# Performance work log

Measured on AMD Instinct MI355X. Metric: run time of the kernel, lower is better.

The kernel has to match this reference:

```python
import jax, jax.numpy as jnp
import numpy as np

EPS = 1e-12
B, C, H, M, E, P = 2, 20000, 64, 8, 200000, 3


def setup_inputs() -> dict:
    key = jax.random.key(0)
    ks = jax.random.split(key, 24)
    inp = {}
    inp["features"] = jax.random.normal(ks[0], (B, C, H), jnp.float32)
    inp["positions"] = jax.random.normal(ks[1], (B, C, P), jnp.float32)
    inp["edge_index"] = jax.random.randint(ks[2], (2, E), 0, C)
    inp["degree"] = jax.random.randint(ks[3], (C,), 1, 33).astype(jnp.float32)
    inp["cell_node_indices"] = jax.random.randint(ks[4], (C, M), 0, C)
    mask = (jax.random.uniform(ks[5], (C, M)) > 0.3).astype(jnp.float32)
    inp["cell_node_mask"] = mask.at[:, 0].set(1.0)  # first node always valid (pad semantics)

    def lin(k, fan_in, fan_out):
        return (jax.random.normal(k, (fan_in, fan_out), jnp.float32) / np.sqrt(fan_in)).astype(jnp.float32)

    # message MLP: Linear(2H+4 -> H), SiLU, Linear(H -> H)
    inp["W1"] = lin(ks[6], 2 * H + 4, H); inp["b1"] = jnp.zeros((H,), jnp.float32)
    inp["W2"] = lin(ks[7], H, H);         inp["b2"] = jnp.zeros((H,), jnp.float32)
    # position MLP: Linear(H -> H), SiLU, Linear(H -> 1)
    inp["P1"] = lin(ks[8], H, H);  inp["pb1"] = jnp.zeros((H,), jnp.float32)
    inp["P2"] = lin(ks[9], H, 1);  inp["pb2"] = jnp.zeros((1,), jnp.float32)
    # update MLP: Linear(2H -> H), SiLU, Linear(H -> H)
    inp["U1"] = lin(ks[10], 2 * H, H); inp["ub1"] = jnp.zeros((H,), jnp.float32)
    inp["U2"] = lin(ks[11], H, H);     inp["ub2"] = jnp.zeros((H,), jnp.float32)
    return inp


def _mlp(x, Wa, ba, Wb, bb):
    return jax.nn.silu(x @ Wa + ba) @ Wb + bb


def _forward(features, positions, edge_index, degree, cell_node_indices, cell_node_mask,
             W1, b1, W2, b2, P1, pb1, P2, pb2, U1, ub1, U2, ub2):
    src, dst = edge_index[0], edge_index[1]
    # gather padded node positions per cell: [B, C, M, P]
    node_pos = positions[:, cell_node_indices]

    h_src = features[:, src]                      # [B,E,H]
    h_dst = features[:, dst]
    rel = positions[:, src] - positions[:, dst]   # [B,E,P]
    dist = jnp.linalg.norm(rel, axis=-1, keepdims=True)  # [B,E,1]

    sp = node_pos[:, src]                         # [B,E,M,P]
    dp = node_pos[:, dst]
    mx = cell_node_mask[src]                      # [E,M]
    my = cell_node_mask[dst]

    # pairwise distances [B,E,M,M] via gram trick (avoids [B,E,M,M,P] intermediate)
    sp2 = jnp.sum(sp * sp, -1)                    # [B,E,M]
    dp2 = jnp.sum(dp * dp, -1)
    cross = jnp.einsum('bemp,benp->bemn', sp, dp)
    d = jnp.sqrt(jnp.maximum(sp2[..., :, None] + dp2[..., None, :] - 2.0 * cross, 0.0) + EPS)

    # masked pairwise-distance sum
    w = mx[:, :, None] * my[:, None, :]           # [E,M,M]
    pairwise = jnp.sum(d * w[None], axis=(-1, -2))  # [B,E]

    # centroid distance
    denx = jnp.maximum(mx.sum(-1, keepdims=True), EPS)  # [E,1]
    deny = jnp.maximum(my.sum(-1, keepdims=True), EPS)
    cx = jnp.sum(sp * mx[None, :, :, None], axis=2) / denx[None]  # [B,E,P]
    cy = jnp.sum(dp * my[None, :, :, None], axis=2) / deny[None]
    centroid = jnp.linalg.norm(cx - cy, axis=-1)  # [B,E]

    # Hausdorff distance (masked min/max)
    inf = jnp.float32(jnp.inf)
    d_xy = jnp.where(my[None, :, None, :] <= 0, inf, d)
    min_xy = jnp.where(mx[None] <= 0, 0.0, d_xy.min(-1))  # [B,E,M]
    h_xy = min_xy.max(-1)                                  # [B,E]
    d_yx = jnp.where(mx[None, :, None, :] <= 0, inf, jnp.swapaxes(d, -1, -2))
    min_yx = jnp.where(my[None] <= 0, 0.0, d_yx.min(-1))
    h_yx = min_yx.max(-1)
    haus = jnp.maximum(h_xy, h_yx)

    invariants = jnp.concatenate([dist, pairwise[..., None], centroid[..., None], haus[..., None]], -1)  # [B,E,4]
    msg_in = jnp.concatenate([h_src, h_dst, invariants], -1)  # [B,E,2H+4]
    messages = _mlp(msg_in, W1, b1, W2, b2)                   # [B,E,H]

    # scatter-aggregate into destination cells, degree-normalize
    agg = jnp.zeros_like(features).at[:, dst].add(messages)
    agg = agg / jnp.maximum(degree, 1.0)[None, :, None]

    # position update
    wts = jnp.tanh(_mlp(messages, P1, pb1, P2, pb2))          # [B,E,1]
    pos_upd = jnp.zeros_like(positions).at[:, dst].add(wts * rel)

    new_features = features + _mlp(jnp.concatenate([features, agg], -1), U1, ub1, U2, ub2)
    new_positions = positions + pos_upd
    return new_features, new_positions


def reference(features, positions, edge_index, degree, cell_node_indices, cell_node_mask,
              W1, b1, W2, b2, P1, pb1, P2, pb2, U1, ub1, U2, ub2):
    return _forward(features, positions, edge_index, degree, cell_node_indices, cell_node_mask,
                    W1, b1, W2, b2, P1, pb1, P2, pb2, U1, ub1, U2, ub2)
```

## Files before the change

kernel.cpp:

```cpp
#include <hip/hip_runtime.h>
#include <hip/hip_bf16.h>

#define B_ 2
#define C_ 20000
#define H_ 64
#define M_ 8
#define E_ 200000
#define P_ 3
#define EPS_ 1e-12f
#define ET_ (E_ / 64)

typedef __attribute__((ext_vector_type(8))) short short8;
typedef __attribute__((ext_vector_type(4))) float float4v;

__device__ __forceinline__ float silu_(float x) {
    return x / (1.f + __expf(-x));
}
__device__ __forceinline__ unsigned short f2b(float f) {
    unsigned u = __float_as_uint(f);
    unsigned r = (u + 0x7FFF + ((u >> 16) & 1)) >> 16;
    return (unsigned short)r;
}
__device__ __forceinline__ float b2f(unsigned short h) {
    return __uint_as_float(((unsigned)h) << 16);
}
__device__ __forceinline__ unsigned pk2u(float a, float b) {
    __hip_bfloat162 h = __float22bfloat162_rn(make_float2(a, b));
    unsigned u; __builtin_memcpy(&u, &h, sizeof(u)); return u;
}

#define W1S_OFF 0
#define W2S_OFF 8192
#define P1S_OFF 12288
#define U1S_OFF 16384
#define U2S_OFF 24576
#define WBUF_ELEMS 28672

#define NB_PREP  120
#define NB_FEATB 2500
#define NB_DESC  157
#define NB_HIST  782
#define NB_COMBO (NB_PREP + NB_FEATB + NB_DESC + NB_HIST)

__global__ __launch_bounds__(256) void combo_kernel(
    const float* __restrict__ W1, const float* __restrict__ W2,
    const float* __restrict__ P1, const float* __restrict__ U1,
    const float* __restrict__ U2, unsigned short* __restrict__ wbuf,
    const float* __restrict__ feat, unsigned short* __restrict__ featb,
    const float* __restrict__ pos, const int* __restrict__ cni,
    const float* __restrict__ mask, float* __restrict__ desc,
    const int* __restrict__ ei, int* __restrict__ cnt)
{
    const int bid = blockIdx.x;
    if (bid < NB_PREP) {
        int t = bid * 256 + threadIdx.x;
        if (t >= WBUF_ELEMS) return;
        const float* W; int e;
        if (t < W2S_OFF)      { W = W1; e = t; }
        else if (t < U1S_OFF) { W = (t < P1S_OFF) ? W2 : P1; e = (t < P1S_OFF) ? t - W2S_OFF : t - P1S_OFF; }
        else if (t < U2S_OFF) { W = U1; e = t - U1S_OFF; }
        else                  { W = U2; e = t - U2S_OFF; }
        int j = e & 7, lane = (e >> 3) & 63, nt = (e >> 9) & 3, kk = e >> 11;
        int k = kk * 32 + ((lane >> 4) * 8) + j;
        int n = nt * 16 + (lane & 15);
        wbuf[t] = f2b(W[k * 64 + n]);
    } else if (bid < NB_PREP + NB_FEATB) {
        int t = (bid - NB_PREP) * 256 + threadIdx.x;
        float4 v = *(const float4*)&feat[(size_t)t * 4];
        *(uint2*)&featb[(size_t)t * 4] = make_uint2(pk2u(v.x, v.y), pk2u(v.z, v.w));
    } else if (bid < NB_PREP + NB_FEATB + NB_DESC) {
        int tid = (bid - NB_PREP - NB_FEATB) * 256 + threadIdx.x;
        if (tid >= B_ * C_) return;
        int b = tid / C_, c = tid - b * C_;
        const float* pb = pos + (size_t)b * C_ * P_;
        float4* D = (float4*)(desc + (size_t)tid * 40);
        int4 n0 = *(const int4*)&cni[c*8];
        int4 n1 = *(const int4*)&cni[c*8 + 4];
        float4 m0 = *(const float4*)&mask[c*8];
        float4 m1 = *(const float4*)&mask[c*8 + 4];
        int ni[8] = {n0.x, n0.y, n0.z, n0.w, n1.x, n1.y, n1.z, n1.w};
        float mm[8] = {m0.x, m0.y, m0.z, m0.w, m1.x, m1.y, m1.z, m1.w};
        float sx = 0.f, sy = 0.f, sz = 0.f, sm = 0.f;
        #pragma unroll
        for (int m = 0; m < 8; ++m) {
            float x = pb[ni[m]*3+0], y = pb[ni[m]*3+1], z = pb[ni[m]*3+2];
            D[m] = make_float4(x, y, z, mm[m]);
            sx += x * mm[m]; sy += y * mm[m]; sz += z * mm[m]; sm += mm[m];
        }
        float inv = 1.f / fmaxf(sm, EPS_);
        D[8] = make_float4(sx * inv, sy * inv, sz * inv, sm);
        D[9] = make_float4(pb[c*3+0], pb[c*3+1], pb[c*3+2], 0.f);
    } else {
        int e = (bid - NB_PREP - NB_FEATB - NB_DESC) * 256 + threadIdx.x;
        if (e >= E_) return;
        atomicAdd(&cnt[ei[E_ + e]], 1);
    }
}

__global__ __launch_bounds__(256) void alloc_kernel(
    const int* __restrict__ cnt, int* __restrict__ cursor, int* __restrict__ total)
{
    int idx = blockIdx.x * 256 + threadIdx.x;
    int lane = threadIdx.x & 63;
    int v = (idx < C_) ? cnt[idx] : 0;
    int inc = v;
    #pragma unroll
    for (int s = 1; s < 64; s <<= 1) {
        int n = __shfl_up(inc, s);
        if (lane >= s) inc += n;
    }
    int wtot = __shfl(inc, 63);
    int base = 0;
    if (lane == 0) base = atomicAdd(total, wtot);
    base = __shfl(base, 0);
    if (idx < C_) cursor[idx] = base + inc - v;
}

__global__ __launch_bounds__(256) void scatter_kernel(
    const int* __restrict__ ei, int* __restrict__ cursor,
    int* __restrict__ ssrc, int* __restrict__ sdst)
{
    int e = blockIdx.x * 256 + threadIdx.x;
    if (e >= E_) return;
    int s = ei[e], d = ei[E_ + e];
    int slot = atomicAdd(&cursor[d], 1);
    ssrc[slot] = s;
    sdst[slot] = d;
}

__global__ __launch_bounds__(256) void edge_kernel(
    const unsigned short* __restrict__ featb,
    const int* __restrict__ ssrc, const int* __restrict__ sdst,
    const float* __restrict__ desc,
    const unsigned short* __restrict__ wbuf, const float* __restrict__ W1,
    const float* __restrict__ b1, const float* __restrict__ b2,
    const float* __restrict__ pb1, const float* __restrict__ P2,
    const float* __restrict__ pb2,
    float* __restrict__ aggf, float* __restrict__ out_pos)
{
    __shared__ unsigned short lds[4 * 3328];

    const int tid  = threadIdx.x;
    const int w    = tid >> 6;
    const int lane = tid & 63;
    const int q    = lane >> 4;
    const int l16  = lane & 15;
    const int w16  = w * 16;

    const int tile = blockIdx.x;
    const int b    = tile / ET_;
    const int i0   = (tile - b * ET_) * 64;
    const int s_l  = ssrc[i0 + lane];
    const int d_l  = sdst[i0 + lane];
    const unsigned short* fb = featb + (size_t)b * C_ * H_;

    unsigned short* Xw = lds + w * 3328;
    unsigned short* Hw = Xw + 2176;
    unsigned short* Mw = Xw;

    const int sg = __shfl(s_l, w16 + l16);
    const int dg = __shfl(d_l, w16 + l16);
    const float4* Ds = (const float4*)(desc + ((size_t)b * C_ + sg) * 40);
    const float4* Dd = (const float4*)(desc + ((size_t)b * C_ + dg) * 40);

    float4 S[8];
    float sp2[8], rowmin[8];
    const float INFV = __builtin_inff();
    #pragma unroll
    for (int i = 0; i < 8; ++i) {
        S[i] = Ds[i];
        sp2[i] = S[i].x*S[i].x + S[i].y*S[i].y + S[i].z*S[i].z;
        rowmin[i] = INFV;
    }
    float pair = 0.f, hyx = 0.f;
    #pragma unroll
    for (int jj = 0; jj < 2; ++jj) {
        float4 Dj = Dd[q*2 + jj];
        float dp2 = Dj.x*Dj.x + Dj.y*Dj.y + Dj.z*Dj.z;
        float colmin = INFV;
        #pragma unroll
        for (int i = 0; i < 8; ++i) {
            float cr = S[i].x*Dj.x + S[i].y*Dj.y + S[i].z*Dj.z;
            float dd = sqrtf(fmaxf(sp2[i] + dp2 - 2.f*cr, 0.f) + EPS_);
            pair += dd * S[i].w * Dj.w;
            rowmin[i] = (Dj.w  > 0.f) ? fminf(rowmin[i], dd) : rowmin[i];
            colmin    = (S[i].w > 0.f) ? fminf(colmin, dd)    : colmin;
        }
        hyx = fmaxf(hyx, (Dj.w > 0.f) ? colmin : 0.f);
    }
    pair += __shfl_xor(pair, 16);  pair += __shfl_xor(pair, 32);
    hyx = fmaxf(hyx, __shfl_xor(hyx, 16));  hyx = fmaxf(hyx, __shfl_xor(hyx, 32));
    #pragma unroll
    for (int i = 0; i < 8; ++i) {
        rowmin[i] = fminf(rowmin[i], __shfl_xor(rowmin[i], 16));
        rowmin[i] = fminf(rowmin[i], __shfl_xor(rowmin[i], 32));
    }
    float hxy = 0.f;
    #pragma unroll
    for (int i = 0; i < 8; ++i)
        hxy = fmaxf(hxy, (S[i].w > 0.f) ? rowmin[i] : 0.f);
    float4 Sc = Ds[8], Dc = Dd[8];
    float cdx = Sc.x - Dc.x, cdy = Sc.y - Dc.y, cdz = Sc.z - Dc.z;
    float4 Sp = Ds[9], Dp = Dd[9];
    const float relx = Sp.x - Dp.x, rely = Sp.y - Dp.y, relz = Sp.z - Dp.z;
    const float ivx = sqrtf(relx*relx + rely*rely + relz*relz);
    const float ivy = pair;
    const float ivz = sqrtf(cdx*cdx + cdy*cdy + cdz*cdz);
    const float ivw = fmaxf(hxy, hyx);

    const int rr4 = lane >> 4, c4 = lane & 15;
    #pragma unroll
    for (int it = 0; it < 4; ++it) {
        int rloc = it * 4 + rr4;
        int r = w16 + rloc;
        int sr = __shfl(s_l, r);
        int dr = __shfl(d_l, r);
        uint2 vs = *(const uint2*)&fb[(size_t)sr * 64 + c4 * 4];
        uint2 vd = *(const uint2*)&fb[(size_t)dr * 64 + c4 * 4];
        *(uint2*)&Xw[rloc*136 + c4*4]      = vs;
        *(uint2*)&Xw[rloc*136 + 64 + c4*4] = vd;
    }

    float4v acc[4];
    #pragma unroll
    for (int nt = 0; nt < 4; ++nt) {
        float bv = b1[nt*16 + l16];
        acc[nt] = (float4v){bv, bv, bv, bv};
    }
    #pragma unroll
    for (int kk = 0; kk < 4; ++kk) {
        short8 a = *(const short8*)&Xw[l16*136 + kk*32 + q*8];
        #pragma unroll
        for (int nt = 0; nt < 4; ++nt) {
            short8 bf = *(const short8*)&wbuf[W1S_OFF + (((kk*4 + nt)*64) + lane) * 8];
            acc[nt] = __builtin_amdgcn_mfma_f32_16x16x32_bf16(a, bf, acc[nt], 0, 0, 0);
        }
    }
    float4 iv[4];
    #pragma unroll
    for (int i = 0; i < 4; ++i) {
        int r = q*4 + i;
        iv[i] = make_float4(__shfl(ivx, r), __shfl(ivy, r),
                            __shfl(ivz, r), __shfl(ivw, r));
    }
    #pragma unroll
    for (int nt = 0; nt < 4; ++nt) {
        float wa = W1[128*64 + nt*16 + l16];
        float wb = W1[129*64 + nt*16 + l16];
        float wc = W1[130*64 + nt*16 + l16];
        float wd = W1[131*64 + nt*16 + l16];
        #pragma unroll
        for (int i = 0; i < 4; ++i)
            acc[nt][i] += iv[i].x*wa + iv[i].y*wb + iv[i].z*wc + iv[i].w*wd;
    }
    #pragma unroll
    for (int nt = 0; nt < 4; ++nt)
        #pragma unroll
        for (int i = 0; i < 4; ++i)
            Hw[(q*4 + i)*72 + nt*16 + l16] = f2b(silu_(acc[nt][i]));

    float4v mac[4];
    #pragma unroll
    for (int nt = 0; nt < 4; ++nt) {
        float bv = b2[nt*16 + l16];
        mac[nt] = (float4v){bv, bv, bv, bv};
    }
    #pragma unroll
    for (int kk = 0; kk < 2; ++kk) {
        short8 a = *(const short8*)&Hw[l16*72 + kk*32 + q*8];
        #pragma unroll
        for (int nt = 0; nt < 4; ++nt) {
            short8 bf = *(const short8*)&wbuf[W2S_OFF + (((kk*4 + nt)*64) + lane) * 8];
            mac[nt] = __builtin_amdgcn_mfma_f32_16x16x32_bf16(a, bf, mac[nt], 0, 0, 0);
        }
    }
    #pragma unroll
    for (int nt = 0; nt < 4; ++nt)
        #pragma unroll
        for (int i = 0; i < 4; ++i)
            Mw[(q*4 + i)*72 + nt*16 + l16] = f2b(mac[nt][i]);

    float4v gac[4];
    #pragma unroll
    for (int nt = 0; nt < 4; ++nt) {
        float bv = pb1[nt*16 + l16];
        gac[nt] = (float4v){bv, bv, bv, bv};
    }
    #pragma unroll
    for (int kk = 0; kk < 2; ++kk) {
        short8 a = *(const short8*)&Mw[l16*72 + kk*32 + q*8];
        #pragma unroll
        for (int nt = 0; nt < 4; ++nt) {
            short8 bf = *(const short8*)&wbuf[P1S_OFF + (((kk*4 + nt)*64) + lane) * 8];
            gac[nt] = __builtin_amdgcn_mfma_f32_16x16x32_bf16(a, bf, gac[nt], 0, 0, 0);
        }
    }
    float p2v[4];
    #pragma unroll
    for (int nt = 0; nt < 4; ++nt) p2v[nt] = P2[nt*16 + l16];
    const float pb2v = pb2[0];

    #pragma unroll
    for (int i = 0; i < 4; ++i) {
        float p = 0.f;
        #pragma unroll
        for (int nt = 0; nt < 4; ++nt) p += silu_(gac[nt][i]) * p2v[nt];
        p += __shfl_xor(p, 8);
        p += __shfl_xor(p, 4);
        p += __shfl_xor(p, 2);
        p += __shfl_xor(p, 1);
        float wt = tanhf(p + pb2v);
        if (l16 == 0) *(float*)&Mw[(q*4 + i)*72 + 64] = wt;
    }

    float mrow[16];
    #pragma unroll
    for (int rr = 0; rr < 16; ++rr) mrow[rr] = b2f(Mw[rr*72 + lane]);
    float wtl = *(const float*)&Mw[l16*72 + 64];

    float* aggB = aggf + (size_t)b * C_ * 64;
    float* opB  = out_pos + (size_t)b * C_ * 3;

    int dprev = __shfl(d_l, w16);
    float colacc = 0.f, pxa = 0.f, pya = 0.f, pza = 0.f;
    #pragma unroll
    for (int rr = 0; rr < 16; ++rr) {
        int dcur = __shfl(d_l, w16 + rr);
        if (dcur != dprev) {
            atomicAdd(&aggB[(size_t)dprev * 64 + lane], colacc);
            if (lane < 3) {
                float v = (lane == 0) ? pxa : (lane == 1) ? pya : pza;
                atomicAdd(&opB[(size_t)dprev * 3 + lane], v);
            }
            colacc = 0.f; pxa = 0.f; pya = 0.f; pza = 0.f;
            dprev = dcur;
        }
        float wt = __shfl(wtl, rr);
        colacc += mrow[rr];
        pxa += wt * __shfl(relx, rr);
        pya += wt * __shfl(rely, rr);
        pza += wt * __shfl(relz, rr);
    }
    atomicAdd(&aggB[(size_t)dprev * 64 + lane], colacc);
    if (lane < 3) {
        float v = (lane == 0) ? pxa : (lane == 1) ? pya : pza;
        atomicAdd(&opB[(size_t)dprev * 3 + lane], v);
    }
}

__global__ __launch_bounds__(256) void node_kernel(
    const float* __restrict__ feat, const unsigned short* __restrict__ featb,
    const float* __restrict__ aggf, const float* __restrict__ deg,
    const unsigned short* __restrict__ wbuf,
    const float* __restrict__ ub1, const float* __restrict__ ub2,
    float* __restrict__ out_feat)
{
    __shared__ unsigned short lds[4 * 3328];

    const int tid  = threadIdx.x;
    const int w    = tid >> 6;
    const int lane = tid & 63;
    const int q    = lane >> 4;
    const int l16  = lane & 15;
    const int g0   = blockIdx.x * 64;

    unsigned short* Xw = lds + w * 3328;
    unsigned short* Hw = Xw + 2176;

    const int rr4 = lane >> 4, c4 = lane & 15;
    #pragma unroll
    for (int it = 0; it < 4; ++it) {
        int rloc = it * 4 + rr4;
        int g = g0 + w*16 + rloc;
        int gc = (g >= C_) ? g - C_ : g;
        float sc = 1.f / fmaxf(deg[gc], 1.f);
        uint2  vf = *(const uint2*)&featb[(size_t)g * 64 + c4 * 4];
        float4 va = *(const float4*)&aggf[(size_t)g * 64 + c4 * 4];
        *(uint2*)&Xw[rloc*136 + c4*4]      = vf;
        *(uint2*)&Xw[rloc*136 + 64 + c4*4] =
            make_uint2(pk2u(va.x*sc, va.y*sc), pk2u(va.z*sc, va.w*sc));
    }

    float4v acc[4];
    #pragma unroll
    for (int nt = 0; nt < 4; ++nt) {
        float bv = ub1[nt*16 + l16];
        acc[nt] = (float4v){bv, bv, bv, bv};
    }
    #pragma unroll
    for (int kk = 0; kk < 4; ++kk) {
        short8 a = *(const short8*)&Xw[l16*136 + kk*32 + q*8];
        #pragma unroll
        for (int nt = 0; nt < 4; ++nt) {
            short8 bf = *(const short8*)&wbuf[U1S_OFF + (((kk*4 + nt)*64) + lane) * 8];
            acc[nt] = __builtin_amdgcn_mfma_f32_16x16x32_bf16(a, bf, acc[nt], 0, 0, 0);
        }
    }
    #pragma unroll
    for (int nt = 0; nt < 4; ++nt)
        #pragma unroll
        for (int i = 0; i < 4; ++i)
            Hw[(q*4 + i)*72 + nt*16 + l16] = f2b(silu_(acc[nt][i]));

    float4v oac[4];
    #pragma unroll
    for (int nt = 0; nt < 4; ++nt) {
        float bv = ub2[nt*16 + l16];
        oac[nt] = (float4v){bv, bv, bv, bv};
    }
    #pragma unroll
    for (int kk = 0; kk < 2; ++kk) {
        short8 a = *(const short8*)&Hw[l16*72 + kk*32 + q*8];
        #pragma unroll
        for (int nt = 0; nt < 4; ++nt) {
            short8 bf = *(const short8*)&wbuf[U2S_OFF + (((kk*4 + nt)*64) + lane) * 8];
            oac[nt] = __builtin_amdgcn_mfma_f32_16x16x32_bf16(a, bf, oac[nt], 0, 0, 0);
        }
    }
    #pragma unroll
    for (int nt = 0; nt < 4; ++nt)
        #pragma unroll
        for (int i = 0; i < 4; ++i) {
            size_t idx = (size_t)(g0 + w*16 + q*4 + i) * 64 + nt*16 + l16;
            out_feat[idx] = feat[idx] + oac[nt][i];
        }
}

extern "C" void kernel_launch(void* const* d_in, const int* in_sizes, int n_in,
                              void* d_out, int out_size, void* d_ws, size_t ws_size,
                              hipStream_t stream) {
    const float* feat = (const float*)d_in[0];
    const float* pos  = (const float*)d_in[1];
    const int*   ei   = (const int*)d_in[2];
    const float* deg  = (const float*)d_in[3];
    const int*   cni  = (const int*)d_in[4];
    const float* mask = (const float*)d_in[5];
    const float* W1   = (const float*)d_in[6];
    const float* b1   = (const float*)d_in[7];
    const float* W2   = (const float*)d_in[8];
    const float* b2   = (const float*)d_in[9];
    const float* P1   = (const float*)d_in[10];
    const float* pb1  = (const float*)d_in[11];
    const float* P2   = (const float*)d_in[12];
    const float* pb2  = (const float*)d_in[13];
    const float* U1   = (const float*)d_in[14];
    const float* ub1  = (const float*)d_in[15];
    const float* U2   = (const float*)d_in[16];
    const float* ub2  = (const float*)d_in[17];

    float* out_feat = (float*)d_out;
    float* out_pos  = out_feat + (size_t)B_ * C_ * H_;

    float* desc = (float*)d_ws;
    float* aggf = desc + (size_t)B_ * C_ * 40;
    unsigned short* featb = (unsigned short*)(aggf + (size_t)B_ * C_ * 64);
    unsigned short* wbuf  = featb + (size_t)B_ * C_ * 64;
    int* cnt    = (int*)(wbuf + WBUF_ELEMS);
    int* total  = cnt + C_;
    int* cursor = total + 1;
    int* ssrc   = cursor + C_;
    int* sdst   = ssrc + E_;

    hipMemsetAsync(cnt, 0, (C_ + 1) * sizeof(int), stream);
    hipMemsetAsync(aggf, 0, (size_t)B_ * C_ * 64 * sizeof(float), stream);
    hipMemcpyAsync(out_pos, pos, (size_t)B_ * C_ * P_ * sizeof(float),
                   hipMemcpyDeviceToDevice, stream);

    combo_kernel<<<NB_COMBO, 256, 0, stream>>>(
        W1, W2, P1, U1, U2, wbuf, feat, featb, pos, cni, mask, desc, ei, cnt);

    alloc_kernel<<<(C_ + 255) / 256, 256, 0, stream>>>(cnt, cursor, total);
    scatter_kernel<<<(E_ + 255) / 256, 256, 0, stream>>>(ei, cursor, ssrc, sdst);

    edge_kernel<<<B_ * ET_, 256, 0, stream>>>(
        featb, ssrc, sdst, desc, wbuf, W1, b1, b2, pb1, P2, pb2, aggf, out_pos);

    node_kernel<<<(B_ * C_) / 64, 256, 0, stream>>>(
        feat, featb, aggf, deg, wbuf, ub1, ub2, out_feat);
}
```

Before: 226.5 us.

## Give each wave its own 64-edge tile in the edge kernel

New measurement: 331.2 us. 1.46x slower.

```diff
diff --git a/kernel.cpp b/kernel.cpp
--- a/kernel.cpp
+++ b/kernel.cpp
@@ -8,7 +8,6 @@
 #define E_ 200000
 #define P_ 3
 #define EPS_ 1e-12f
-#define ET_ (E_ / 64)
 
 typedef __attribute__((ext_vector_type(8))) short short8;
 typedef __attribute__((ext_vector_type(4))) float float4v;
@@ -36,11 +35,11 @@
 #define U2S_OFF 24576
 #define WBUF_ELEMS 28672
 
-#define NB_PREP  120
-#define NB_FEATB 2500
-#define NB_DESC  157
-#define NB_HIST  782
-#define NB_COMBO (NB_PREP + NB_FEATB + NB_DESC + NB_HIST)
+#define NB_PREP   120
+#define NB_FEATB  2500
+#define NB_DESC   157
+#define NB_HIST   782
+#define NB_COMBO  (NB_PREP + NB_FEATB + NB_DESC + NB_HIST)
 
 __global__ __launch_bounds__(256) void combo_kernel(
     const float* __restrict__ W1, const float* __restrict__ W2,
@@ -118,19 +117,18 @@
 
 __global__ __launch_bounds__(256) void scatter_kernel(
     const int* __restrict__ ei, int* __restrict__ cursor,
-    int* __restrict__ ssrc, int* __restrict__ sdst)
+    int2* __restrict__ sedge)
 {
     int e = blockIdx.x * 256 + threadIdx.x;
     if (e >= E_) return;
     int s = ei[e], d = ei[E_ + e];
     int slot = atomicAdd(&cursor[d], 1);
-    ssrc[slot] = s;
-    sdst[slot] = d;
-}
-
-__global__ __launch_bounds__(256) void edge_kernel(
+    sedge[slot] = make_int2(s, d);
+}
+
+__global__ __launch_bounds__(128, 4) void edge_kernel(
     const unsigned short* __restrict__ featb,
-    const int* __restrict__ ssrc, const int* __restrict__ sdst,
+    const int2* __restrict__ sedge,
     const float* __restrict__ desc,
     const unsigned short* __restrict__ wbuf, const float* __restrict__ W1,
     const float* __restrict__ b1, const float* __restrict__ b2,
@@ -138,62 +136,59 @@
     const float* __restrict__ pb2,
     float* __restrict__ aggf, float* __restrict__ out_pos)
 {
-    __shared__ unsigned short lds[4 * 3328];
+    __shared__ __align__(16) unsigned short lds[2 * 4352];
 
     const int tid  = threadIdx.x;
     const int w    = tid >> 6;
     const int lane = tid & 63;
     const int q    = lane >> 4;
     const int l16  = lane & 15;
-    const int w16  = w * 16;
-
-    const int tile = blockIdx.x;
-    const int b    = tile / ET_;
-    const int i0   = (tile - b * ET_) * 64;
-    const int s_l  = ssrc[i0 + lane];
-    const int d_l  = sdst[i0 + lane];
+
+    const int wid  = blockIdx.x * 2 + w;
+    const int b    = wid / (E_ / 64);
+    const int i0   = (wid - b * (E_ / 64)) * 64;
+
+    const int2 sd  = sedge[i0 + lane];
+    const int s_l  = sd.x;
+    const int d_l  = sd.y;
     const unsigned short* fb = featb + (size_t)b * C_ * H_;
 
-    unsigned short* Xw = lds + w * 3328;
+    unsigned short* Xw = lds + w * 4352;
     unsigned short* Hw = Xw + 2176;
     unsigned short* Mw = Xw;
-
-    const int sg = __shfl(s_l, w16 + l16);
-    const int dg = __shfl(d_l, w16 + l16);
-    const float4* Ds = (const float4*)(desc + ((size_t)b * C_ + sg) * 40);
-    const float4* Dd = (const float4*)(desc + ((size_t)b * C_ + dg) * 40);
-
-    float4 S[8];
-    float sp2[8], rowmin[8];
+    float* IVw = (float*)(Xw + 3328);
+
+    const float4* Ds = (const float4*)(desc + ((size_t)b * C_ + s_l) * 40);
+    const float4* Dd = (const float4*)(desc + ((size_t)b * C_ + d_l) * 40);
     const float INFV = __builtin_inff();
+    float4 S[8], D[8];
+    #pragma unroll
+    for (int i = 0; i < 8; ++i) { S[i] = Ds[i]; D[i] = Dd[i]; }
+    float a_i[8], infm_i[8], rowmin[8];
     #pragma unroll
     for (int i = 0; i < 8; ++i) {
-        S[i] = Ds[i];
-        sp2[i] = S[i].x*S[i].x + S[i].y*S[i].y + S[i].z*S[i].z;
+        a_i[i] = S[i].x*S[i].x + S[i].y*S[i].y + S[i].z*S[i].z + EPS_;
+        infm_i[i] = (S[i].w > 0.f) ? 0.f : INFV;
         rowmin[i] = INFV;
     }
     float pair = 0.f, hyx = 0.f;
     #pragma unroll
-    for (int jj = 0; jj < 2; ++jj) {
-        float4 Dj = Dd[q*2 + jj];
+    for (int j = 0; j < 8; ++j) {
+        float4 Dj = D[j];
         float dp2 = Dj.x*Dj.x + Dj.y*Dj.y + Dj.z*Dj.z;
-        float colmin = INFV;
+        float infm_j = (Dj.w > 0.f) ? 0.f : INFV;
+        float colmin = INFV, psum = 0.f;
         #pragma unroll
         for (int i = 0; i < 8; ++i) {
             float cr = S[i].x*Dj.x + S[i].y*Dj.y + S[i].z*Dj.z;
-            float dd = sqrtf(fmaxf(sp2[i] + dp2 - 2.f*cr, 0.f) + EPS_);
-            pair += dd * S[i].w * Dj.w;
-            rowmin[i] = (Dj.w  > 0.f) ? fminf(rowmin[i], dd) : rowmin[i];
-            colmin    = (S[i].w > 0.f) ? fminf(colmin, dd)    : colmin;
-        }
+            float t  = (a_i[i] + dp2) - 2.f*cr;
+            float dd = sqrtf(fmaxf(t, EPS_));
+            psum = fmaf(dd, S[i].w, psum);
+            rowmin[i] = fminf(rowmin[i], dd + infm_j);
+            colmin    = fminf(colmin,    dd + infm_i[i]);
+        }
+        pair = fmaf(Dj.w, psum, pair);
         hyx = fmaxf(hyx, (Dj.w > 0.f) ? colmin : 0.f);
-    }
-    pair += __shfl_xor(pair, 16);  pair += __shfl_xor(pair, 32);
-    hyx = fmaxf(hyx, __shfl_xor(hyx, 16));  hyx = fmaxf(hyx, __shfl_xor(hyx, 32));
-    #pragma unroll
-    for (int i = 0; i < 8; ++i) {
-        rowmin[i] = fminf(rowmin[i], __shfl_xor(rowmin[i], 16));
-        rowmin[i] = fminf(rowmin[i], __shfl_xor(rowmin[i], 32));
     }
     float hxy = 0.f;
     #pragma unroll
@@ -203,148 +198,144 @@
     float cdx = Sc.x - Dc.x, cdy = Sc.y - Dc.y, cdz = Sc.z - Dc.z;
     float4 Sp = Ds[9], Dp = Dd[9];
     const float relx = Sp.x - Dp.x, rely = Sp.y - Dp.y, relz = Sp.z - Dp.z;
-    const float ivx = sqrtf(relx*relx + rely*rely + relz*relz);
-    const float ivy = pair;
-    const float ivz = sqrtf(cdx*cdx + cdy*cdy + cdz*cdz);
-    const float ivw = fmaxf(hxy, hyx);
-
-    const int rr4 = lane >> 4, c4 = lane & 15;
-    #pragma unroll
-    for (int it = 0; it < 4; ++it) {
-        int rloc = it * 4 + rr4;
-        int r = w16 + rloc;
-        int sr = __shfl(s_l, r);
-        int dr = __shfl(d_l, r);
-        uint2 vs = *(const uint2*)&fb[(size_t)sr * 64 + c4 * 4];
-        uint2 vd = *(const uint2*)&fb[(size_t)dr * 64 + c4 * 4];
-        *(uint2*)&Xw[rloc*136 + c4*4]      = vs;
-        *(uint2*)&Xw[rloc*136 + 64 + c4*4] = vd;
-    }
-
-    float4v acc[4];
+    {
+        float ivx = sqrtf(relx*relx + rely*rely + relz*relz);
+        float ivz = sqrtf(cdx*cdx + cdy*cdy + cdz*cdz);
+        float ivw = fmaxf(hxy, hyx);
+        *(float4*)&IVw[lane*8]     = make_float4(ivx, pair, ivz, ivw);
+        *(float4*)&IVw[lane*8 + 4] = make_float4(relx, rely, relz, 0.f);
+    }
+
+    float b1v[4], b2v[4], pb1v[4], p2v[4];
+    float wta[4], wtb[4], wtc[4], wtd[4];
     #pragma unroll
     for (int nt = 0; nt < 4; ++nt) {
-        float bv = b1[nt*16 + l16];
-        acc[nt] = (float4v){bv, bv, bv, bv};
-    }
-    #pragma unroll
-    for (int kk = 0; kk < 4; ++kk) {
-        short8 a = *(const short8*)&Xw[l16*136 + kk*32 + q*8];
-        #pragma unroll
-        for (int nt = 0; nt < 4; ++nt) {
-            short8 bf = *(const short8*)&wbuf[W1S_OFF + (((kk*4 + nt)*64) + lane) * 8];
-            acc[nt] = __builtin_amdgcn_mfma_f32_16x16x32_bf16(a, bf, acc[nt], 0, 0, 0);
-        }
-    }
-    float4 iv[4];
-    #pragma unroll
-    for (int i = 0; i < 4; ++i) {
-        int r = q*4 + i;
-        iv[i] = make_float4(__shfl(ivx, r), __shfl(ivy, r),
-                            __shfl(ivz, r), __shfl(ivw, r));
-    }
-    #pragma unroll
-    for (int nt = 0; nt < 4; ++nt) {
-        float wa = W1[128*64 + nt*16 + l16];
-        float wb = W1[129*64 + nt*16 + l16];
-        float wc = W1[130*64 + nt*16 + l16];
-        float wd = W1[131*64 + nt*16 + l16];
-        #pragma unroll
-        for (int i = 0; i < 4; ++i)
-            acc[nt][i] += iv[i].x*wa + iv[i].y*wb + iv[i].z*wc + iv[i].w*wd;
-    }
-    #pragma unroll
-    for (int nt = 0; nt < 4; ++nt)
-        #pragma unroll
-        for (int i = 0; i < 4; ++i)
-            Hw[(q*4 + i)*72 + nt*16 + l16] = f2b(silu_(acc[nt][i]));
-
-    float4v mac[4];
-    #pragma unroll
-    for (int nt = 0; nt < 4; ++nt) {
-        float bv = b2[nt*16 + l16];
-        mac[nt] = (float4v){bv, bv, bv, bv};
-    }
-    #pragma unroll
-    for (int kk = 0; kk < 2; ++kk) {
-        short8 a = *(const short8*)&Hw[l16*72 + kk*32 + q*8];
-        #pragma unroll
-        for (int nt = 0; nt < 4; ++nt) {
-            short8 bf = *(const short8*)&wbuf[W2S_OFF + (((kk*4 + nt)*64) + lane) * 8];
-            mac[nt] = __builtin_amdgcn_mfma_f32_16x16x32_bf16(a, bf, mac[nt], 0, 0, 0);
-        }
-    }
-    #pragma unroll
-    for (int nt = 0; nt < 4; ++nt)
-        #pragma unroll
-        for (int i = 0; i < 4; ++i)
-            Mw[(q*4 + i)*72 + nt*16 + l16] = f2b(mac[nt][i]);
-
-    float4v gac[4];
-    #pragma unroll
-    for (int nt = 0; nt < 4; ++nt) {
-        float bv = pb1[nt*16 + l16];
-        gac[nt] = (float4v){bv, bv, bv, bv};
-    }
-    #pragma unroll
-    for (int kk = 0; kk < 2; ++kk) {
-        short8 a = *(const short8*)&Mw[l16*72 + kk*32 + q*8];
-        #pragma unroll
-        for (int nt = 0; nt < 4; ++nt) {
-            short8 bf = *(const short8*)&wbuf[P1S_OFF + (((kk*4 + nt)*64) + lane) * 8];
-            gac[nt] = __builtin_amdgcn_mfma_f32_16x16x32_bf16(a, bf, gac[nt], 0, 0, 0);
-        }
-    }
-    float p2v[4];
-    #pragma unroll
-    for (int nt = 0; nt < 4; ++nt) p2v[nt] = P2[nt*16 + l16];
+        b1v[nt]  = b1[nt*16 + l16];
+        b2v[nt]  = b2[nt*16 + l16];
+        pb1v[nt] = pb1[nt*16 + l16];
+        p2v[nt]  = P2[nt*16 + l16];
+        wta[nt]  = W1[128*64 + nt*16 + l16];
+        wtb[nt]  = W1[129*64 + nt*16 + l16];
+        wtc[nt]  = W1[130*64 + nt*16 + l16];
+        wtd[nt]  = W1[131*64 + nt*16 + l16];
+    }
     const float pb2v = pb2[0];
-
-    #pragma unroll
-    for (int i = 0; i < 4; ++i) {
-        float p = 0.f;
-        #pragma unroll
-        for (int nt = 0; nt < 4; ++nt) p += silu_(gac[nt][i]) * p2v[nt];
-        p += __shfl_xor(p, 8);
-        p += __shfl_xor(p, 4);
-        p += __shfl_xor(p, 2);
-        p += __shfl_xor(p, 1);
-        float wt = tanhf(p + pb2v);
-        if (l16 == 0) *(float*)&Mw[(q*4 + i)*72 + 64] = wt;
-    }
-
-    float mrow[16];
-    #pragma unroll
-    for (int rr = 0; rr < 16; ++rr) mrow[rr] = b2f(Mw[rr*72 + lane]);
-    float wtl = *(const float*)&Mw[l16*72 + 64];
 
     float* aggB = aggf + (size_t)b * C_ * 64;
     float* opB  = out_pos + (size_t)b * C_ * 3;
-
-    int dprev = __shfl(d_l, w16);
-    float colacc = 0.f, pxa = 0.f, pya = 0.f, pza = 0.f;
-    #pragma unroll
-    for (int rr = 0; rr < 16; ++rr) {
-        int dcur = __shfl(d_l, w16 + rr);
-        if (dcur != dprev) {
-            atomicAdd(&aggB[(size_t)dprev * 64 + lane], colacc);
-            if (lane < 3) {
-                float v = (lane == 0) ? pxa : (lane == 1) ? pya : pza;
-                atomicAdd(&opB[(size_t)dprev * 3 + lane], v);
+    const int rr4 = lane >> 4, c4 = lane & 15;
+
+    for (int it = 0; it < 4; ++it) {
+        #pragma unroll
+        for (int it2 = 0; it2 < 4; ++it2) {
+            int rloc = it2 * 4 + rr4;
+            int sr = __shfl(s_l, it*16 + rloc);
+            int dr = __shfl(d_l, it*16 + rloc);
+            *(uint2*)&Xw[rloc*136 + c4*4]      = *(const uint2*)&fb[(size_t)sr*64 + c4*4];
+            *(uint2*)&Xw[rloc*136 + 64 + c4*4] = *(const uint2*)&fb[(size_t)dr*64 + c4*4];
+        }
+
+        float4v acc[4];
+        #pragma unroll
+        for (int nt = 0; nt < 4; ++nt)
+            acc[nt] = (float4v){b1v[nt], b1v[nt], b1v[nt], b1v[nt]};
+        #pragma unroll
+        for (int kk = 0; kk < 4; ++kk) {
+            short8 a = *(const short8*)&Xw[l16*136 + kk*32 + q*8];
+            #pragma unroll
+            for (int nt = 0; nt < 4; ++nt) {
+                short8 bf = *(const short8*)&wbuf[W1S_OFF + (((kk*4 + nt)*64) + lane) * 8];
+                acc[nt] = __builtin_amdgcn_mfma_f32_16x16x32_bf16(a, bf, acc[nt], 0, 0, 0);
             }
-            colacc = 0.f; pxa = 0.f; pya = 0.f; pza = 0.f;
-            dprev = dcur;
-        }
-        float wt = __shfl(wtl, rr);
-        colacc += mrow[rr];
-        pxa += wt * __shfl(relx, rr);
-        pya += wt * __shfl(rely, rr);
-        pza += wt * __shfl(relz, rr);
-    }
-    atomicAdd(&aggB[(size_t)dprev * 64 + lane], colacc);
-    if (lane < 3) {
-        float v = (lane == 0) ? pxa : (lane == 1) ? pya : pza;
-        atomicAdd(&opB[(size_t)dprev * 3 + lane], v);
+        }
+        #pragma unroll
+        for (int i = 0; i < 4; ++i) {
+            float4 iv = *(const float4*)&IVw[(it*16 + q*4 + i) * 8];
+            #pragma unroll
+            for (int nt = 0; nt < 4; ++nt)
+                acc[nt][i] += iv.x*wta[nt] + iv.y*wtb[nt] + iv.z*wtc[nt] + iv.w*wtd[nt];
+        }
+        #pragma unroll
+        for (int nt = 0; nt < 4; ++nt)
+            #pragma unroll
+            for (int i = 0; i < 4; ++i)
+                Hw[(q*4 + i)*72 + nt*16 + l16] = f2b(silu_(acc[nt][i]));
+
+        float4v mac[4];
+        #pragma unroll
+        for (int nt = 0; nt < 4; ++nt)
+            mac[nt] = (float4v){b2v[nt], b2v[nt], b2v[nt], b2v[nt]};
+        #pragma unroll
+        for (int kk = 0; kk < 2; ++kk) {
+            short8 a = *(const short8*)&Hw[l16*72 + kk*32 + q*8];
+            #pragma unroll
+            for (int nt = 0; nt < 4; ++nt) {
+                short8 bf = *(const short8*)&wbuf[W2S_OFF + (((kk*4 + nt)*64) + lane) * 8];
+                mac[nt] = __builtin_amdgcn_mfma_f32_16x16x32_bf16(a, bf, mac[nt], 0, 0, 0);
+            }
+        }
+        #pragma unroll
+        for (int nt = 0; nt < 4; ++nt)
+            #pragma unroll
+            for (int i = 0; i < 4; ++i)
+                Mw[(q*4 + i)*72 + nt*16 + l16] = f2b(mac[nt][i]);
+
+        float4v gac[4];
+        #pragma unroll
+        for (int nt = 0; nt < 4; ++nt)
+            gac[nt] = (float4v){pb1v[nt], pb1v[nt], pb1v[nt], pb1v[nt]};
+        #pragma unroll
+        for (int kk = 0; kk < 2; ++kk) {
+            short8 a = *(const short8*)&Mw[l16*72 + kk*32 + q*8];
+            #pragma unroll
+            for (int nt = 0; nt < 4; ++nt) {
+                short8 bf = *(const short8*)&wbuf[P1S_OFF + (((kk*4 + nt)*64) + lane) * 8];
+                gac[nt] = __builtin_amdgcn_mfma_f32_16x16x32_bf16(a, bf, gac[nt], 0, 0, 0);
+            }
+        }
+        #pragma unroll
+        for (int i = 0; i < 4; ++i) {
+            float p = 0.f;
+            #pragma unroll
+            for (int nt = 0; nt < 4; ++nt) p += silu_(gac[nt][i]) * p2v[nt];
+            p += __shfl_xor(p, 8);
+            p += __shfl_xor(p, 4);
+            p += __shfl_xor(p, 2);
+            p += __shfl_xor(p, 1);
+            float wt = tanhf(p + pb2v);
+            if (l16 == 0) *(float*)&Mw[(q*4 + i)*72 + 64] = wt;
+        }
+
+        float mrow[16];
+        #pragma unroll
+        for (int rr = 0; rr < 16; ++rr) mrow[rr] = b2f(Mw[rr*72 + lane]);
+        float wtl = *(const float*)&Mw[l16*72 + 64];
+
+        int dprev = __shfl(d_l, it*16);
+        float colacc = 0.f, pxa = 0.f, pya = 0.f, pza = 0.f;
+        #pragma unroll
+        for (int rr = 0; rr < 16; ++rr) {
+            int dcur = __shfl(d_l, it*16 + rr);
+            if (dcur != dprev) {
+                atomicAdd(&aggB[(size_t)dprev * 64 + lane], colacc);
+                if (lane < 3) {
+                    float v = (lane == 0) ? pxa : (lane == 1) ? pya : pza;
+                    atomicAdd(&opB[(size_t)dprev * 3 + lane], v);
+                }
+                colacc = 0.f; pxa = 0.f; pya = 0.f; pza = 0.f;
+                dprev = dcur;
+            }
+            float wt = __shfl(wtl, rr);
+            colacc += mrow[rr];
+            pxa = fmaf(wt, __shfl(relx, it*16 + rr), pxa);
+            pya = fmaf(wt, __shfl(rely, it*16 + rr), pya);
+            pza = fmaf(wt, __shfl(relz, it*16 + rr), pza);
+        }
+        atomicAdd(&aggB[(size_t)dprev * 64 + lane], colacc);
+        if (lane < 3) {
+            float v = (lane == 0) ? pxa : (lane == 1) ? pya : pza;
+            atomicAdd(&opB[(size_t)dprev * 3 + lane], v);
+        }
     }
 }
 
@@ -458,8 +449,7 @@
     int* cnt    = (int*)(wbuf + WBUF_ELEMS);
     int* total  = cnt + C_;
     int* cursor = total + 1;
-    int* ssrc   = cursor + C_;
-    int* sdst   = ssrc + E_;
+    int2* sedge = (int2*)(cursor + C_);
 
     hipMemsetAsync(cnt, 0, (C_ + 1) * sizeof(int), stream);
     hipMemsetAsync(aggf, 0, (size_t)B_ * C_ * 64 * sizeof(float), stream);
@@ -470,10 +460,10 @@
         W1, W2, P1, U1, U2, wbuf, feat, featb, pos, cni, mask, desc, ei, cnt);
 
     alloc_kernel<<<(C_ + 255) / 256, 256, 0, stream>>>(cnt, cursor, total);
-    scatter_kernel<<<(E_ + 255) / 256, 256, 0, stream>>>(ei, cursor, ssrc, sdst);
-
-    edge_kernel<<<B_ * ET_, 256, 0, stream>>>(
-        featb, ssrc, sdst, desc, wbuf, W1, b1, b2, pb1, P2, pb2, aggf, out_pos);
+    scatter_kernel<<<(E_ + 255) / 256, 256, 0, stream>>>(ei, cursor, sedge);
+
+    edge_kernel<<<(B_ * E_) / 128, 128, 0, stream>>>(
+        featb, sedge, desc, wbuf, W1, b1, b2, pb1, P2, pb2, aggf, out_pos);
 
     node_kernel<<<(B_ * C_) / 64, 256, 0, stream>>>(
         feat, featb, aggf, deg, wbuf, ub1, ub2, out_feat);
```

## Split edge geometry into a separate per-edge kernel and fuse memset/copy into it

Applied to the files above, without the earlier changes.

Result: slower. 247.3 us (+9.2%).

```diff
diff --git a/kernel.cpp b/kernel.cpp
--- a/kernel.cpp
+++ b/kernel.cpp
@@ -16,6 +16,10 @@
 __device__ __forceinline__ float silu_(float x) {
     return x / (1.f + __expf(-x));
 }
+__device__ __forceinline__ float tanh_fast_(float x) {
+    float ex = __expf(2.f * x);
+    return 1.f - 2.f / (ex + 1.f);
+}
 __device__ __forceinline__ unsigned short f2b(float f) {
     unsigned u = __float_as_uint(f);
     unsigned r = (u + 0x7FFF + ((u >> 16) & 1)) >> 16;
@@ -36,11 +40,16 @@
 #define U2S_OFF 24576
 #define WBUF_ELEMS 28672
 
-#define NB_PREP  120
-#define NB_FEATB 2500
-#define NB_DESC  157
-#define NB_HIST  782
-#define NB_COMBO (NB_PREP + NB_FEATB + NB_DESC + NB_HIST)
+#define NB_PREP   120
+#define NB_FEATB  2500
+#define NB_DESC   157
+#define NB_HIST   782
+#define NB_COMBO  (NB_PREP + NB_FEATB + NB_DESC + NB_HIST)
+
+#define NB_GEOM   3125
+#define NB_AGGZ   2500
+#define NB_PCPY   118
+#define NB_GEOMK  (NB_GEOM + NB_AGGZ + NB_PCPY)
 
 __global__ __launch_bounds__(256) void combo_kernel(
     const float* __restrict__ W1, const float* __restrict__ W2,
@@ -118,20 +127,85 @@
 
 __global__ __launch_bounds__(256) void scatter_kernel(
     const int* __restrict__ ei, int* __restrict__ cursor,
-    int* __restrict__ ssrc, int* __restrict__ sdst)
+    int2* __restrict__ sedge)
 {
     int e = blockIdx.x * 256 + threadIdx.x;
     if (e >= E_) return;
     int s = ei[e], d = ei[E_ + e];
     int slot = atomicAdd(&cursor[d], 1);
-    ssrc[slot] = s;
-    sdst[slot] = d;
+    sedge[slot] = make_int2(s, d);
+}
+
+__global__ __launch_bounds__(256) void geom_kernel(
+    const int2* __restrict__ sedge, const float* __restrict__ desc,
+    float* __restrict__ inv8,
+    float* __restrict__ aggf, const float* __restrict__ pos,
+    float* __restrict__ out_pos)
+{
+    const int bid = blockIdx.x;
+    if (bid >= NB_GEOM) {
+        if (bid < NB_GEOM + NB_AGGZ) {
+            int t = (bid - NB_GEOM) * 256 + threadIdx.x;
+            ((float4*)aggf)[t] = make_float4(0.f, 0.f, 0.f, 0.f);
+        } else {
+            int t = (bid - NB_GEOM - NB_AGGZ) * 256 + threadIdx.x;
+            if (t < (B_ * C_ * P_) / 4)
+                ((float4*)out_pos)[t] = ((const float4*)pos)[t];
+        }
+        return;
+    }
+    int gid = bid * 256 + threadIdx.x;
+    int b = gid / E_, i = gid - b * E_;
+    int2 sd = sedge[i];
+    const float4* Ds = (const float4*)(desc + ((size_t)b * C_ + sd.x) * 40);
+    const float4* Dd = (const float4*)(desc + ((size_t)b * C_ + sd.y) * 40);
+    const float INFV = __builtin_inff();
+    float4 S[8];
+    float a_i[8], infm_i[8], rowmin[8];
+    #pragma unroll
+    for (int k = 0; k < 8; ++k) {
+        S[k] = Ds[k];
+        a_i[k] = S[k].x*S[k].x + S[k].y*S[k].y + S[k].z*S[k].z + EPS_;
+        infm_i[k] = (S[k].w > 0.f) ? 0.f : INFV;
+        rowmin[k] = INFV;
+    }
+    float pair = 0.f, hyx = 0.f;
+    #pragma unroll
+    for (int j = 0; j < 8; ++j) {
+        float4 Dj = Dd[j];
+        float dp2 = Dj.x*Dj.x + Dj.y*Dj.y + Dj.z*Dj.z;
+        float infm_j = (Dj.w > 0.f) ? 0.f : INFV;
+        float colmin = INFV, psum = 0.f;
+        #pragma unroll
+        for (int k = 0; k < 8; ++k) {
+            float cr = S[k].x*Dj.x + S[k].y*Dj.y + S[k].z*Dj.z;
+            float t  = (a_i[k] + dp2) - 2.f*cr;
+            float dd = sqrtf(fmaxf(t, EPS_));
+            psum = fmaf(dd, S[k].w, psum);
+            rowmin[k] = fminf(rowmin[k], dd + infm_j);
+            colmin    = fminf(colmin,    dd + infm_i[k]);
+        }
+        pair = fmaf(Dj.w, psum, pair);
+        hyx = fmaxf(hyx, (Dj.w > 0.f) ? colmin : 0.f);
+    }
+    float hxy = 0.f;
+    #pragma unroll
+    for (int k = 0; k < 8; ++k)
+        hxy = fmaxf(hxy, (S[k].w > 0.f) ? rowmin[k] : 0.f);
+    float4 Sc = Ds[8], Dc = Dd[8];
+    float cdx = Sc.x - Dc.x, cdy = Sc.y - Dc.y, cdz = Sc.z - Dc.z;
+    float4 Sp = Ds[9], Dp = Dd[9];
+    float relx = Sp.x - Dp.x, rely = Sp.y - Dp.y, relz = Sp.z - Dp.z;
+    float dist = sqrtf(relx*relx + rely*rely + relz*relz);
+    float cen  = sqrtf(cdx*cdx + cdy*cdy + cdz*cdz);
+    float haus = fmaxf(hxy, hyx);
+    ((float4*)inv8)[(size_t)gid * 2]     = make_float4(dist, pair, cen, haus);
+    ((float4*)inv8)[(size_t)gid * 2 + 1] = make_float4(relx, rely, relz, 0.f);
 }
 
 __global__ __launch_bounds__(256) void edge_kernel(
     const unsigned short* __restrict__ featb,
-    const int* __restrict__ ssrc, const int* __restrict__ sdst,
-    const float* __restrict__ desc,
+    const int2* __restrict__ sedge, const float* __restrict__ inv8,
     const unsigned short* __restrict__ wbuf, const float* __restrict__ W1,
     const float* __restrict__ b1, const float* __restrict__ b2,
     const float* __restrict__ pb1, const float* __restrict__ P2,
@@ -150,63 +224,18 @@
     const int tile = blockIdx.x;
     const int b    = tile / ET_;
     const int i0   = (tile - b * ET_) * 64;
-    const int s_l  = ssrc[i0 + lane];
-    const int d_l  = sdst[i0 + lane];
+    const int2 sd  = sedge[i0 + lane];
+    const int s_l  = sd.x;
+    const int d_l  = sd.y;
     const unsigned short* fb = featb + (size_t)b * C_ * H_;
+    const float* ivb = inv8 + ((size_t)b * E_ + i0) * 8;
 
     unsigned short* Xw = lds + w * 3328;
     unsigned short* Hw = Xw + 2176;
     unsigned short* Mw = Xw;
 
-    const int sg = __shfl(s_l, w16 + l16);
-    const int dg = __shfl(d_l, w16 + l16);
-    const float4* Ds = (const float4*)(desc + ((size_t)b * C_ + sg) * 40);
-    const float4* Dd = (const float4*)(desc + ((size_t)b * C_ + dg) * 40);
-
-    float4 S[8];
-    float sp2[8], rowmin[8];
-    const float INFV = __builtin_inff();
-    #pragma unroll
-    for (int i = 0; i < 8; ++i) {
-        S[i] = Ds[i];
-        sp2[i] = S[i].x*S[i].x + S[i].y*S[i].y + S[i].z*S[i].z;
-        rowmin[i] = INFV;
-    }
-    float pair = 0.f, hyx = 0.f;
-    #pragma unroll
-    for (int jj = 0; jj < 2; ++jj) {
-        float4 Dj = Dd[q*2 + jj];
-        float dp2 = Dj.x*Dj.x + Dj.y*Dj.y + Dj.z*Dj.z;
-        float colmin = INFV;
-        #pragma unroll
-        for (int i = 0; i < 8; ++i) {
-            float cr = S[i].x*Dj.x + S[i].y*Dj.y + S[i].z*Dj.z;
-            float dd = sqrtf(fmaxf(sp2[i] + dp2 - 2.f*cr, 0.f) + EPS_);
-            pair += dd * S[i].w * Dj.w;
-            rowmin[i] = (Dj.w  > 0.f) ? fminf(rowmin[i], dd) : rowmin[i];
-            colmin    = (S[i].w > 0.f) ? fminf(colmin, dd)    : colmin;
-        }
-        hyx = fmaxf(hyx, (Dj.w > 0.f) ? colmin : 0.f);
-    }
-    pair += __shfl_xor(pair, 16);  pair += __shfl_xor(pair, 32);
-    hyx = fmaxf(hyx, __shfl_xor(hyx, 16));  hyx = fmaxf(hyx, __shfl_xor(hyx, 32));
-    #pragma unroll
-    for (int i = 0; i < 8; ++i) {
-        rowmin[i] = fminf(rowmin[i], __shfl_xor(rowmin[i], 16));
-        rowmin[i] = fminf(rowmin[i], __shfl_xor(rowmin[i], 32));
-    }
-    float hxy = 0.f;
-    #pragma unroll
-    for (int i = 0; i < 8; ++i)
-        hxy = fmaxf(hxy, (S[i].w > 0.f) ? rowmin[i] : 0.f);
-    float4 Sc = Ds[8], Dc = Dd[8];
-    float cdx = Sc.x - Dc.x, cdy = Sc.y - Dc.y, cdz = Sc.z - Dc.z;
-    float4 Sp = Ds[9], Dp = Dd[9];
-    const float relx = Sp.x - Dp.x, rely = Sp.y - Dp.y, relz = Sp.z - Dp.z;
-    const float ivx = sqrtf(relx*relx + rely*rely + relz*relz);
-    const float ivy = pair;
-    const float ivz = sqrtf(cdx*cdx + cdy*cdy + cdz*cdz);
-    const float ivw = fmaxf(hxy, hyx);
+    float4 ivhi = *(const float4*)&ivb[(w16 + l16) * 8 + 4];
+    const float relx = ivhi.x, rely = ivhi.y, relz = ivhi.z;
 
     const int rr4 = lane >> 4, c4 = lane & 15;
     #pragma unroll
@@ -238,11 +267,8 @@
     }
     float4 iv[4];
     #pragma unroll
-    for (int i = 0; i < 4; ++i) {
-        int r = q*4 + i;
-        iv[i] = make_float4(__shfl(ivx, r), __shfl(ivy, r),
-                            __shfl(ivz, r), __shfl(ivw, r));
-    }
+    for (int i = 0; i < 4; ++i)
+        iv[i] = *(const float4*)&ivb[(w16 + q*4 + i) * 8];
     #pragma unroll
     for (int nt = 0; nt < 4; ++nt) {
         float wa = W1[128*64 + nt*16 + l16];
@@ -309,17 +335,17 @@
         p += __shfl_xor(p, 4);
         p += __shfl_xor(p, 2);
         p += __shfl_xor(p, 1);
-        float wt = tanhf(p + pb2v);
+        float wt = tanh_fast_(p + pb2v);
         if (l16 == 0) *(float*)&Mw[(q*4 + i)*72 + 64] = wt;
     }
+
+    float* aggB = aggf + (size_t)b * C_ * 64;
+    float* opB  = out_pos + (size_t)b * C_ * 3;
 
     float mrow[16];
     #pragma unroll
     for (int rr = 0; rr < 16; ++rr) mrow[rr] = b2f(Mw[rr*72 + lane]);
     float wtl = *(const float*)&Mw[l16*72 + 64];
-
-    float* aggB = aggf + (size_t)b * C_ * 64;
-    float* opB  = out_pos + (size_t)b * C_ * 3;
 
     int dprev = __shfl(d_l, w16);
     float colacc = 0.f, pxa = 0.f, pya = 0.f, pza = 0.f;
@@ -337,9 +363,9 @@
         }
         float wt = __shfl(wtl, rr);
         colacc += mrow[rr];
-        pxa += wt * __shfl(relx, rr);
-        pya += wt * __shfl(rely, rr);
-        pza += wt * __shfl(relz, rr);
+        pxa = fmaf(wt, __shfl(relx, rr), pxa);
+        pya = fmaf(wt, __shfl(rely, rr), pya);
+        pza = fmaf(wt, __shfl(relz, rr), pza);
     }
     atomicAdd(&aggB[(size_t)dprev * 64 + lane], colacc);
     if (lane < 3) {
@@ -457,23 +483,22 @@
     unsigned short* wbuf  = featb + (size_t)B_ * C_ * 64;
     int* cnt    = (int*)(wbuf + WBUF_ELEMS);
     int* total  = cnt + C_;
-    int* cursor = total + 1;
-    int* ssrc   = cursor + C_;
-    int* sdst   = ssrc + E_;
-
-    hipMemsetAsync(cnt, 0, (C_ + 1) * sizeof(int), stream);
-    hipMemsetAsync(aggf, 0, (size_t)B_ * C_ * 64 * sizeof(float), stream);
-    hipMemcpyAsync(out_pos, pos, (size_t)B_ * C_ * P_ * sizeof(float),
-                   hipMemcpyDeviceToDevice, stream);
+    int* cursor = total + 4;
+    int2* sedge = (int2*)(cursor + C_);
+    float* inv8 = (float*)(sedge + E_);
+
+    hipMemsetAsync(cnt, 0, (C_ + 4) * sizeof(int), stream);
 
     combo_kernel<<<NB_COMBO, 256, 0, stream>>>(
         W1, W2, P1, U1, U2, wbuf, feat, featb, pos, cni, mask, desc, ei, cnt);
 
     alloc_kernel<<<(C_ + 255) / 256, 256, 0, stream>>>(cnt, cursor, total);
-    scatter_kernel<<<(E_ + 255) / 256, 256, 0, stream>>>(ei, cursor, ssrc, sdst);
+    scatter_kernel<<<(E_ + 255) / 256, 256, 0, stream>>>(ei, cursor, sedge);
+
+    geom_kernel<<<NB_GEOMK, 256, 0, stream>>>(sedge, desc, inv8, aggf, pos, out_pos);
 
     edge_kernel<<<B_ * ET_, 256, 0, stream>>>(
-        featb, ssrc, sdst, desc, wbuf, W1, b1, b2, pb1, P2, pb2, aggf, out_pos);
+        featb, sedge, inv8, wbuf, W1, b1, b2, pb1, P2, pb2, aggf, out_pos);
 
     node_kernel<<<(B_ * C_) / 64, 256, 0, stream>>>(
         feat, featb, aggf, deg, wbuf, ub1, ub2, out_feat);
```
